# Performance work log

Measured on AMD Instinct MI355X. Metric: run time of the kernel, lower is better.

Reference implementation:

```python
import jax, jax.numpy as jnp
import numpy as np

N_PTS = 65536
N_VERTS = 6890
N_JOINTS = 24


def build_rotation(q):
    # q: [N,4] unnormalized quaternion (r, x, y, z) -> [N,3,3] rotation matrix
    q = q / jnp.linalg.norm(q, axis=-1, keepdims=True)
    r, x, y, z = q[:, 0], q[:, 1], q[:, 2], q[:, 3]
    R = jnp.stack([
        1 - 2 * (y * y + z * z), 2 * (x * y - r * z), 2 * (x * z + r * y),
        2 * (x * y + r * z), 1 - 2 * (x * x + z * z), 2 * (y * z - r * x),
        2 * (x * z - r * y), 2 * (y * z + r * x), 1 - 2 * (x * x + y * y),
    ], axis=-1).reshape(-1, 3, 3)
    return R


def setup_inputs() -> dict:
    key = jax.random.key(0)
    k1, k2, k3, k4, k5 = jax.random.split(key, 5)
    xyz = jax.random.normal(k1, (N_PTS, 3), dtype=jnp.float32)
    rotation = jax.random.normal(k2, (N_PTS, 4), dtype=jnp.float32)
    smpl_verts = jax.random.normal(k3, (N_VERTS, 3), dtype=jnp.float32)
    skinning_weights = jax.random.uniform(k4, (N_VERTS, N_JOINTS), dtype=jnp.float32)
    # row-normalize like real LBS weights
    skinning_weights = skinning_weights / jnp.sum(skinning_weights, axis=-1, keepdims=True)
    bone_transforms = jax.random.normal(k5, (N_JOINTS, 4, 4), dtype=jnp.float32)
    return {"xyz": xyz, "rotation": rotation, "smpl_verts": smpl_verts,
            "skinning_weights": skinning_weights, "bone_transforms": bone_transforms}


def reference(xyz, rotation, smpl_verts, skinning_weights, bone_transforms):
    # --- 1-NN brute-force search (knn_points with K=1) ---
    d2 = (jnp.sum(xyz * xyz, axis=-1, keepdims=True)
          - 2.0 * (xyz @ smpl_verts.T)
          + jnp.sum(smpl_verts * smpl_verts, axis=-1)[None, :])
    p_idx = jnp.argmin(d2, axis=-1)                      # [N]

    # --- skinning-weight gather ---
    pts_W = skinning_weights[p_idx]                      # [N, 24]

    # --- LBS: blend bone transforms ---
    T_fwd = (pts_W @ bone_transforms.reshape(-1, 16)).reshape(-1, 4, 4)  # [N,4,4]

    # --- transform points (homogeneous) ---
    x_bar = jnp.einsum('nij,nj->ni', T_fwd[:, :3, :3], xyz) + T_fwd[:, :3, 3]  # [N,3]

    # --- rotate covariance rotations ---
    rotation_hat = build_rotation(rotation)              # [N,3,3]
    rotation_bar = jnp.einsum('nij,njk->nik', T_fwd[:, :3, :3], rotation_hat)  # [N,3,3]

    return (x_bar, rotation_bar, T_fwd)
```

## Files before the change

kernel.cpp:

```cpp
#include <hip/hip_runtime.h>
#include <math.h>

#define NPTS 65536
#define NV 6890
#define NT 432
#define NTPAD 8
#define VSPLIT 4
#define TILES_PER_WAVE (NT / VSPLIT)
#define NJ 24
#define PTS_PER_BLK 32
#define NBLK (NPTS / PTS_PER_BLK)

typedef double f64x4 __attribute__((ext_vector_type(4)));

__global__ void prep_frags_k(const float* __restrict__ verts, double* __restrict__ bf) {
    int e = blockIdx.x * blockDim.x + threadIdx.x;
    if (e >= (NT + NTPAD) * 64) return;
    int l = e & 63;
    int t = e >> 6;
    int j = t * 16 + (l & 15);
    int k = l >> 4;
    double val;
    if (j < NV) {
        if (k < 3) {
            val = (double)verts[3 * j + k];
        } else {
            double x = (double)verts[3 * j + 0];
            double y = (double)verts[3 * j + 1];
            double z = (double)verts[3 * j + 2];
            val = x * x + y * y + z * z;
        }
    } else {
        val = (k == 3) ? 1e300 : 0.0;
    }
    bf[e] = val;
}

__device__ __forceinline__ double packdt(double d, int t) {
    unsigned long long u = __double_as_longlong(d);
    u = (u & ~0xFFULL) | (unsigned long long)(unsigned)t;
    return __longlong_as_double(u);
}

__launch_bounds__(256)
__global__ void smplnn_main(const float* __restrict__ xyz,
                            const float* __restrict__ rot,
                            const double* __restrict__ bf,
                            const float* __restrict__ sw,
                            const float* __restrict__ bt,
                            float* __restrict__ out) {
    __shared__ double smin[VSPLIT][2][16][16];

    const int tid  = threadIdx.x;
    const int lane = tid & 63;
    const int wave = tid >> 6;
    const int r = lane & 15;
    const int k = lane >> 4;
    const int pbase = blockIdx.x * PTS_PER_BLK;

    double a0 = (k == 3) ? 1.0 : -2.0 * (double)xyz[3 * (pbase + r) + k];
    double a1 = (k == 3) ? 1.0 : -2.0 * (double)xyz[3 * (pbase + 16 + r) + k];

    const f64x4 zero = {0.0, 0.0, 0.0, 0.0};

    double ar  = (k == 3) ? (double)r : 0.0;
    double one = (k == 3) ? 1.0 : 0.0;
    f64x4 drow = __builtin_amdgcn_mfma_f64_16x16x4f64(ar, one, zero, 0, 0, 0);
    f64x4 dcol = __builtin_amdgcn_mfma_f64_16x16x4f64(one, ar, zero, 0, 0, 0);
    int rowid[4], colid[4];
    #pragma unroll
    for (int v = 0; v < 4; ++v) { rowid[v] = (int)drow[v]; colid[v] = (int)dcol[v]; }

    double m0[4], m1[4];
    #pragma unroll
    for (int v = 0; v < 4; ++v) { m0[v] = 1e301; m1[v] = 1e301; }

    const int tbase = wave * TILES_PER_WAVE;
    const double* bl = bf + (size_t)tbase * 64 + lane;
    double bcur = bl[0];
    #pragma unroll 4
    for (int t = 0; t < TILES_PER_WAVE; ++t) {
        double bnext = bl[(size_t)(t + 1) * 64];
        f64x4 d0 = __builtin_amdgcn_mfma_f64_16x16x4f64(a0, bcur, zero, 0, 0, 0);
        f64x4 d1 = __builtin_amdgcn_mfma_f64_16x16x4f64(a1, bcur, zero, 0, 0, 0);
        #pragma unroll
        for (int v = 0; v < 4; ++v) {
            m0[v] = fmin(m0[v], packdt(d0[v], t));
            m1[v] = fmin(m1[v], packdt(d1[v], t));
        }
        bcur = bnext;
    }

    #pragma unroll
    for (int v = 0; v < 4; ++v) {
        smin[wave][0][rowid[v]][colid[v]] = m0[v];
        smin[wave][1][rowid[v]][colid[v]] = m1[v];
    }
    __syncthreads();

    if (wave != 0 || lane >= 32) return;
    const int set  = lane >> 4;
    const int prow = lane & 15;
    const int i = pbase + set * 16 + prow;

    double best = 1e302;
    int bw = 0, bc = 0;
    #pragma unroll
    for (int w = 0; w < VSPLIT; ++w) {
        #pragma unroll
        for (int c = 0; c < 16; ++c) {
            double bv = smin[w][set][prow][c];
            if (bv < best) { best = bv; bw = w; bc = c; }
        }
    }
    const int tl = (int)(__double_as_longlong(best) & 0xFFULL);
    const int bi = (bw * TILES_PER_WAVE + tl) * 16 + bc;

    const float xf = xyz[3 * i + 0];
    const float yf = xyz[3 * i + 1];
    const float zf = xyz[3 * i + 2];

    const float* W = &sw[bi * NJ];
    float Tm[16];
    #pragma unroll
    for (int q = 0; q < 16; ++q) Tm[q] = 0.0f;
    #pragma unroll
    for (int kk = 0; kk < NJ; ++kk) {
        float w = W[kk];
        #pragma unroll
        for (int q = 0; q < 16; ++q) Tm[q] = fmaf(w, bt[16 * kk + q], Tm[q]);
    }

    float xb0 = Tm[0] * xf + Tm[1] * yf + Tm[2]  * zf + Tm[3];
    float xb1 = Tm[4] * xf + Tm[5] * yf + Tm[6]  * zf + Tm[7];
    float xb2 = Tm[8] * xf + Tm[9] * yf + Tm[10] * zf + Tm[11];

    float qr = rot[4 * i + 0];
    float qx = rot[4 * i + 1];
    float qy = rot[4 * i + 2];
    float qz = rot[4 * i + 3];
    float inv = 1.0f / sqrtf(qr * qr + qx * qx + qy * qy + qz * qz);
    qr *= inv; qx *= inv; qy *= inv; qz *= inv;

    float Rh[9];
    Rh[0] = 1.0f - 2.0f * (qy * qy + qz * qz);
    Rh[1] = 2.0f * (qx * qy - qr * qz);
    Rh[2] = 2.0f * (qx * qz + qr * qy);
    Rh[3] = 2.0f * (qx * qy + qr * qz);
    Rh[4] = 1.0f - 2.0f * (qx * qx + qz * qz);
    Rh[5] = 2.0f * (qy * qz - qr * qx);
    Rh[6] = 2.0f * (qx * qz - qr * qy);
    Rh[7] = 2.0f * (qy * qz + qr * qx);
    Rh[8] = 1.0f - 2.0f * (qx * qx + qy * qy);

    float RB[9];
    #pragma unroll
    for (int rr = 0; rr < 3; ++rr) {
        #pragma unroll
        for (int cc = 0; cc < 3; ++cc) {
            RB[3 * rr + cc] = Tm[4 * rr + 0] * Rh[cc]
                            + Tm[4 * rr + 1] * Rh[3 + cc]
                            + Tm[4 * rr + 2] * Rh[6 + cc];
        }
    }

    out[3 * i + 0] = xb0;
    out[3 * i + 1] = xb1;
    out[3 * i + 2] = xb2;
    float* ob = out + 3 * NPTS + 9 * i;
    #pragma unroll
    for (int q = 0; q < 9; ++q) ob[q] = RB[q];
    float* ot = out + 12 * NPTS + 16 * i;
    #pragma unroll
    for (int q = 0; q < 16; ++q) ot[q] = Tm[q];
}

extern "C" void kernel_launch(void* const* d_in, const int* in_sizes, int n_in,
                              void* d_out, int out_size, void* d_ws, size_t ws_size,
                              hipStream_t stream) {
    const float* xyz   = (const float*)d_in[0];
    const float* rot   = (const float*)d_in[1];
    const float* verts = (const float*)d_in[2];
    const float* sw    = (const float*)d_in[3];
    const float* bt    = (const float*)d_in[4];
    float* out = (float*)d_out;

    double* bfrag = (double*)d_ws;
    prep_frags_k<<<((NT + NTPAD) * 64 + 255) / 256, 256, 0, stream>>>(verts, bfrag);
    smplnn_main<<<NBLK, 256, 0, stream>>>(xyz, rot, bfrag, sw, bt, out);
}
```

Measured before the change: 137.6 us.

## Process 64 points per block and pack full vertex index into mantissa

Doubles the points per block so each loaded vertex fragment feeds four MFMA tiles instead of two, halving B-fragment traffic per point and the number of blocks. The loop is manually unrolled by two with a two-deep prefetch. The low 13 mantissa bits now carry the global vertex index, so the final reduction becomes a branchless fmin and the epilogue uses a full wave. The cost is more accumulator registers, fewer blocks in flight, and tie-breaking and precision now depending on 13 truncated bits.

Result: faster. 120.9 us (-12.1%).

```diff
diff --git a/kernel.cpp b/kernel.cpp
--- a/kernel.cpp
+++ b/kernel.cpp
@@ -8,7 +8,7 @@
 #define VSPLIT 4
 #define TILES_PER_WAVE (NT / VSPLIT)
 #define NJ 24
-#define PTS_PER_BLK 32
+#define PTS_PER_BLK 64
 #define NBLK (NPTS / PTS_PER_BLK)
 
 typedef double f64x4 __attribute__((ext_vector_type(4)));
@@ -36,9 +36,9 @@
     bf[e] = val;
 }
 
-__device__ __forceinline__ double packdt(double d, int t) {
+__device__ __forceinline__ double packdx(double d, unsigned orv) {
     unsigned long long u = __double_as_longlong(d);
-    u = (u & ~0xFFULL) | (unsigned long long)(unsigned)t;
+    u = (u & ~0x1FFFULL) | (unsigned long long)orv;
     return __longlong_as_double(u);
 }
 
@@ -49,7 +49,7 @@
                             const float* __restrict__ sw,
                             const float* __restrict__ bt,
                             float* __restrict__ out) {
-    __shared__ double smin[VSPLIT][2][16][16];
+    __shared__ double smin[VSPLIT][4][16][16];
 
     const int tid  = threadIdx.x;
     const int lane = tid & 63;
@@ -58,8 +58,10 @@
     const int k = lane >> 4;
     const int pbase = blockIdx.x * PTS_PER_BLK;
 
-    double a0 = (k == 3) ? 1.0 : -2.0 * (double)xyz[3 * (pbase + r) + k];
+    double a0 = (k == 3) ? 1.0 : -2.0 * (double)xyz[3 * (pbase +      r) + k];
     double a1 = (k == 3) ? 1.0 : -2.0 * (double)xyz[3 * (pbase + 16 + r) + k];
+    double a2 = (k == 3) ? 1.0 : -2.0 * (double)xyz[3 * (pbase + 32 + r) + k];
+    double a3 = (k == 3) ? 1.0 : -2.0 * (double)xyz[3 * (pbase + 48 + r) + k];
 
     const f64x4 zero = {0.0, 0.0, 0.0, 0.0};
 
@@ -67,54 +69,79 @@
     double one = (k == 3) ? 1.0 : 0.0;
     f64x4 drow = __builtin_amdgcn_mfma_f64_16x16x4f64(ar, one, zero, 0, 0, 0);
     f64x4 dcol = __builtin_amdgcn_mfma_f64_16x16x4f64(one, ar, zero, 0, 0, 0);
-    int rowid[4], colid[4];
-    #pragma unroll
-    for (int v = 0; v < 4; ++v) { rowid[v] = (int)drow[v]; colid[v] = (int)dcol[v]; }
-
-    double m0[4], m1[4];
-    #pragma unroll
-    for (int v = 0; v < 4; ++v) { m0[v] = 1e301; m1[v] = 1e301; }
+    int rowid[4];
+    unsigned colb[4];
+    #pragma unroll
+    for (int v = 0; v < 4; ++v) { rowid[v] = (int)drow[v]; colb[v] = (unsigned)(int)dcol[v]; }
+
+    double m0[4], m1[4], m2[4], m3[4];
+    #pragma unroll
+    for (int v = 0; v < 4; ++v) { m0[v] = 1e301; m1[v] = 1e301; m2[v] = 1e301; m3[v] = 1e301; }
 
     const int tbase = wave * TILES_PER_WAVE;
     const double* bl = bf + (size_t)tbase * 64 + lane;
-    double bcur = bl[0];
-    #pragma unroll 4
-    for (int t = 0; t < TILES_PER_WAVE; ++t) {
-        double bnext = bl[(size_t)(t + 1) * 64];
-        f64x4 d0 = __builtin_amdgcn_mfma_f64_16x16x4f64(a0, bcur, zero, 0, 0, 0);
-        f64x4 d1 = __builtin_amdgcn_mfma_f64_16x16x4f64(a1, bcur, zero, 0, 0, 0);
-        #pragma unroll
-        for (int v = 0; v < 4; ++v) {
-            m0[v] = fmin(m0[v], packdt(d0[v], t));
-            m1[v] = fmin(m1[v], packdt(d1[v], t));
-        }
-        bcur = bnext;
+    double b0 = bl[0];
+    double b1 = bl[64];
+    for (int t = 0; t < TILES_PER_WAVE; t += 2) {
+        double p0 = bl[(size_t)(t + 2) * 64];
+        double p1 = bl[(size_t)(t + 3) * 64];
+        {
+            const unsigned tb = (unsigned)((tbase + t) << 4);
+            f64x4 d0 = __builtin_amdgcn_mfma_f64_16x16x4f64(a0, b0, zero, 0, 0, 0);
+            f64x4 d1 = __builtin_amdgcn_mfma_f64_16x16x4f64(a1, b0, zero, 0, 0, 0);
+            f64x4 d2 = __builtin_amdgcn_mfma_f64_16x16x4f64(a2, b0, zero, 0, 0, 0);
+            f64x4 d3 = __builtin_amdgcn_mfma_f64_16x16x4f64(a3, b0, zero, 0, 0, 0);
+            #pragma unroll
+            for (int v = 0; v < 4; ++v) {
+                const unsigned orv = tb | colb[v];
+                m0[v] = fmin(m0[v], packdx(d0[v], orv));
+                m1[v] = fmin(m1[v], packdx(d1[v], orv));
+                m2[v] = fmin(m2[v], packdx(d2[v], orv));
+                m3[v] = fmin(m3[v], packdx(d3[v], orv));
+            }
+        }
+        {
+            const unsigned tb = (unsigned)((tbase + t + 1) << 4);
+            f64x4 d0 = __builtin_amdgcn_mfma_f64_16x16x4f64(a0, b1, zero, 0, 0, 0);
+            f64x4 d1 = __builtin_amdgcn_mfma_f64_16x16x4f64(a1, b1, zero, 0, 0, 0);
+            f64x4 d2 = __builtin_amdgcn_mfma_f64_16x16x4f64(a2, b1, zero, 0, 0, 0);
+            f64x4 d3 = __builtin_amdgcn_mfma_f64_16x16x4f64(a3, b1, zero, 0, 0, 0);
+            #pragma unroll
+            for (int v = 0; v < 4; ++v) {
+                const unsigned orv = tb | colb[v];
+                m0[v] = fmin(m0[v], packdx(d0[v], orv));
+                m1[v] = fmin(m1[v], packdx(d1[v], orv));
+                m2[v] = fmin(m2[v], packdx(d2[v], orv));
+                m3[v] = fmin(m3[v], packdx(d3[v], orv));
+            }
+        }
+        b0 = p0;
+        b1 = p1;
     }
 
     #pragma unroll
     for (int v = 0; v < 4; ++v) {
-        smin[wave][0][rowid[v]][colid[v]] = m0[v];
-        smin[wave][1][rowid[v]][colid[v]] = m1[v];
+        smin[wave][0][rowid[v]][colb[v]] = m0[v];
+        smin[wave][1][rowid[v]][colb[v]] = m1[v];
+        smin[wave][2][rowid[v]][colb[v]] = m2[v];
+        smin[wave][3][rowid[v]][colb[v]] = m3[v];
     }
     __syncthreads();
 
-    if (wave != 0 || lane >= 32) return;
-    const int set  = lane >> 4;
-    const int prow = lane & 15;
-    const int i = pbase + set * 16 + prow;
+    if (wave != 0) return;
+    const int set = lane >> 4;
+    const int row = lane & 15;
+    const int i = pbase + lane;
 
     double best = 1e302;
-    int bw = 0, bc = 0;
     #pragma unroll
     for (int w = 0; w < VSPLIT; ++w) {
         #pragma unroll
         for (int c = 0; c < 16; ++c) {
-            double bv = smin[w][set][prow][c];
-            if (bv < best) { best = bv; bw = w; bc = c; }
-        }
-    }
-    const int tl = (int)(__double_as_longlong(best) & 0xFFULL);
-    const int bi = (bw * TILES_PER_WAVE + tl) * 16 + bc;
+            best = fmin(best, smin[w][set][row][c]);
+        }
+    }
+    const int bi = (int)(__double_as_longlong(best) & 0x1FFFULL);
 
     const float xf = xyz[3 * i + 0];
     const float yf = xyz[3 * i + 1];
```
